# Kernel tuning notes

Hardware: AMD Instinct MI355X
Metric: run time of the kernel (lower is better)

The kernel has to match this reference:

```python
import jax, jax.numpy as jnp
import numpy as np

N_NODES = 50000
N_EDGES = 800000
NODE_IN = 256
EDGE_OUT = 64
GLOBAL_IN = 128
NODE_OUT = 256
HIDDEN = 512
N_GRAPHS = 64


def setup_inputs() -> dict:
    key = jax.random.key(0)
    ks = jax.random.split(key, 8)
    x = jax.random.normal(ks[0], (N_NODES, NODE_IN), dtype=jnp.float32)
    edge_index = jax.random.randint(ks[1], (2, N_EDGES), 0, N_NODES, dtype=jnp.int64)
    edge_attr = jax.random.normal(ks[2], (N_EDGES, EDGE_OUT), dtype=jnp.float32)
    u = jax.random.normal(ks[3], (N_GRAPHS, GLOBAL_IN), dtype=jnp.float32)
    batch = jnp.sort(jax.random.randint(ks[4], (N_NODES,), 0, N_GRAPHS, dtype=jnp.int64))
    in_dim = NODE_IN + EDGE_OUT + GLOBAL_IN
    # MLP params (torch nn.Linear default init: U(-1/sqrt(fan_in), 1/sqrt(fan_in)))
    b1s = 1.0 / np.sqrt(in_dim)
    b2s = 1.0 / np.sqrt(HIDDEN)
    W1 = jax.random.uniform(ks[5], (in_dim, HIDDEN), dtype=jnp.float32, minval=-b1s, maxval=b1s)
    b1 = jnp.zeros((HIDDEN,), dtype=jnp.float32)
    W2 = jax.random.uniform(ks[6], (HIDDEN, NODE_OUT), dtype=jnp.float32, minval=-b2s, maxval=b2s)
    b2 = jnp.zeros((NODE_OUT,), dtype=jnp.float32)
    return {"x": x, "edge_index": edge_index, "edge_attr": edge_attr, "u": u,
            "batch": batch, "W1": W1, "b1": b1, "W2": W2, "b2": b2}


def reference(x, edge_index, edge_attr, u, batch, W1, b1, W2, b2):
    n = x.shape[0]
    src = edge_index[0]
    # scatter_mean(edge_attr, src, dim=0, dim_size=n)
    sums = jax.ops.segment_sum(edge_attr, src, num_segments=n)          # [N, E_out]
    counts = jax.ops.segment_sum(jnp.ones((edge_attr.shape[0],), edge_attr.dtype),
                                 src, num_segments=n)                   # [N]
    edge_attr_agg = sums / jnp.maximum(counts, 1.0)[:, None]
    u_expanded = u[batch]                                               # [N, G_in]
    combined = jnp.concatenate([x, edge_attr_agg, u_expanded], axis=1)  # [N, 448]
    h = jax.nn.relu(combined @ W1 + b1)                                 # [N, H]
    return h @ W2 + b2                                                  # [N, N_out]
```

## Files before the change

### kernel.cpp

```cpp
#include <hip/hip_runtime.h>
#include <hip/hip_bf16.h>
#include <stdint.h>

#define NN 50000
#define NE 800000
#define NODE_IN 256
#define EDGE_OUT 64
#define GLOBAL_IN 128
#define NODE_OUT 256
#define HIDDEN 512
#define K1 320
#define N_GRAPHS 64
#define MAXDEG 64

typedef __attribute__((ext_vector_type(8))) short bf16x8;
typedef __attribute__((ext_vector_type(4))) float f32x4;
typedef __attribute__((ext_vector_type(4))) unsigned short us4;

__device__ __forceinline__ unsigned short f2bf(float x) {
    union { float f; unsigned int u; } c; c.f = x;
    unsigned int u = c.u;
    unsigned int r = (u + 0x7FFFu + ((u >> 16) & 1u)) >> 16;
    return (unsigned short)r;
}

#define GLD_LDS(gp, lp) __builtin_amdgcn_global_load_lds( \
    (const __attribute__((address_space(1))) unsigned int*)(gp), \
    (__attribute__((address_space(3))) unsigned int*)(lp), 16, 0, 0)

#define PREP_W1 (HIDDEN * K1)
#define PREP_W2 (PREP_W1 + NODE_OUT * HIDDEN)
#define PREP_G  (PREP_W2 + N_GRAPHS * HIDDEN)
#define PREP_Z  (PREP_G + NN)
__global__ __launch_bounds__(256)
void prep(const float* __restrict__ W1, const float* __restrict__ W2,
          const float* __restrict__ u, const float* __restrict__ b1,
          unsigned short* __restrict__ W1T, unsigned short* __restrict__ W2T,
          float* __restrict__ G, int* __restrict__ cnt)
{
    int idx = blockIdx.x * 256 + threadIdx.x;
    if (idx < PREP_W1) {
        int n = idx / K1, k = idx - n * K1;
        W1T[idx] = f2bf(W1[(size_t)k * HIDDEN + n]);
    } else if (idx < PREP_W2) {
        int j = idx - PREP_W1;
        int n = j / HIDDEN, k = j - n * HIDDEN;
        W2T[j] = f2bf(W2[(size_t)k * NODE_OUT + n]);
    } else if (idx < PREP_G) {
        int j = idx - PREP_W2;
        int g = j >> 9, col = j & 511;
        const float* up = u + (size_t)g * GLOBAL_IN;
        float acc = b1[col];
        #pragma unroll 4
        for (int k = 0; k < GLOBAL_IN; ++k)
            acc += up[k] * W1[(size_t)(K1 + k) * HIDDEN + col];
        G[j] = acc;
    } else if (idx < PREP_Z) {
        cnt[idx - PREP_G] = 0;
    }
}

__global__ __launch_bounds__(256)
void fill_perm(const int* __restrict__ src, int* __restrict__ cnt,
               int* __restrict__ perm)
{
    int e = blockIdx.x * 256 + threadIdx.x;
    if (e < NE) {
        int s = src[e];
        int pos = atomicAdd(&cnt[s], 1);
        if (pos < MAXDEG) perm[(size_t)s * MAXDEG + pos] = e;
    }
}

__global__ __launch_bounds__(256)
void seg_comb(const float* __restrict__ edge_attr,
              const int* __restrict__ perm,
              const int* __restrict__ cnt,
              const float* __restrict__ x,
              unsigned short* __restrict__ comb)
{
    int node = blockIdx.x * 4 + (threadIdx.x >> 6);
    if (node >= NN) return;
    int lane = threadIdx.x & 63;
    unsigned short* crow = comb + (size_t)node * K1;

    {
        const float4 v = *(const float4*)(x + (size_t)node * NODE_IN + lane * 4);
        us4 o = { f2bf(v.x), f2bf(v.y), f2bf(v.z), f2bf(v.w) };
        *(us4*)(crow + lane * 4) = o;
    }
    int c = cnt[node];
    int cc = c < MAXDEG ? c : MAXDEG;
    int g = lane >> 4;
    int f = (lane & 15) * 4;
    const int* pbase = perm + (size_t)node * MAXDEG;
    float4 acc = make_float4(0.f, 0.f, 0.f, 0.f);
    for (int i = g; i < cc; i += 4) {
        int e = pbase[i];
        const float4 v = *(const float4*)(edge_attr + (size_t)e * EDGE_OUT + f);
        acc.x += v.x; acc.y += v.y; acc.z += v.z; acc.w += v.w;
    }
    #pragma unroll
    for (int off = 16; off < 64; off <<= 1) {
        acc.x += __shfl_xor(acc.x, off, 64);
        acc.y += __shfl_xor(acc.y, off, 64);
        acc.z += __shfl_xor(acc.z, off, 64);
        acc.w += __shfl_xor(acc.w, off, 64);
    }
    if (g == 0) {
        float inv = 1.0f / fmaxf((float)c, 1.0f);
        us4 o = { f2bf(acc.x * inv), f2bf(acc.y * inv),
                  f2bf(acc.z * inv), f2bf(acc.w * inv) };
        *(us4*)(crow + NODE_IN + f) = o;
    }
}

template<int EPI>
__global__ __launch_bounds__(256)
void gemm_bt_128(const unsigned short* __restrict__ A,
                 const unsigned short* __restrict__ B,
                 const float* __restrict__ bias,
                 const int* __restrict__ batch,
                 void* __restrict__ Cv,
                 int M, int N, int K)
{
    __shared__ unsigned short lA[128 * 32];
    __shared__ unsigned short lB[128 * 32];
    const int tid = threadIdx.x;
    const int w = tid >> 6, l = tid & 63;
    const int m0 = blockIdx.y * 128;
    const int n0 = blockIdx.x * 128;
    const int wr = w >> 1, wc = w & 1;

    f32x4 acc[4][4] = {};

    const int cA0 = w * 64 + l;
    const int cA1 = (w + 4) * 64 + l;
    const int rA0 = cA0 >> 2, kA0 = (cA0 & 3) * 8;
    const int rA1 = cA1 >> 2, kA1 = (cA1 & 3) * 8;
    int gr0 = m0 + rA0; if (gr0 >= M) gr0 = M - 1;
    int gr1 = m0 + rA1; if (gr1 >= M) gr1 = M - 1;
    const unsigned short* pA0 = A + (size_t)gr0 * K + kA0;
    const unsigned short* pA1 = A + (size_t)gr1 * K + kA1;
    const unsigned short* pB0 = B + (size_t)(n0 + rA0) * K + kA0;
    const unsigned short* pB1 = B + (size_t)(n0 + rA1) * K + kA1;

    for (int k0 = 0; k0 < K; k0 += 32) {
        GLD_LDS(pA0 + k0, &lA[(size_t)cA0 * 8]);
        GLD_LDS(pA1 + k0, &lA[(size_t)cA1 * 8]);
        GLD_LDS(pB0 + k0, &lB[(size_t)cA0 * 8]);
        GLD_LDS(pB1 + k0, &lB[(size_t)cA1 * 8]);
        __syncthreads();

        bf16x8 af[4], bfr[4];
        #pragma unroll
        for (int m = 0; m < 4; ++m)
            af[m] = *(const bf16x8*)&lA[(wr * 64 + m * 16 + (l & 15)) * 32 + (l >> 4) * 8];
        #pragma unroll
        for (int n = 0; n < 4; ++n)
            bfr[n] = *(const bf16x8*)&lB[(wc * 64 + n * 16 + (l & 15)) * 32 + (l >> 4) * 8];

        #pragma unroll
        for (int m = 0; m < 4; ++m)
            #pragma unroll
            for (int n = 0; n < 4; ++n)
                acc[m][n] = __builtin_amdgcn_mfma_f32_16x16x32_bf16(af[m], bfr[n], acc[m][n], 0, 0, 0);

        __syncthreads();
    }

    const int cbase = n0 + wc * 64 + (l & 15);
    const int rbase = m0 + wr * 64 + ((l >> 4) << 2);
    if (EPI == 0) {
        unsigned short* C = (unsigned short*)Cv;
        #pragma unroll
        for (int m = 0; m < 4; ++m) {
            #pragma unroll
            for (int j = 0; j < 4; ++j) {
                int row = rbase + m * 16 + j;
                if (row < M) {
                    const float* grow = bias + (size_t)batch[row] * HIDDEN;
                    #pragma unroll
                    for (int n = 0; n < 4; ++n) {
                        int c = cbase + n * 16;
                        float v = acc[m][n][j] + grow[c];
                        v = fmaxf(v, 0.0f);
                        C[(size_t)row * N + c] = f2bf(v);
                    }
                }
            }
        }
    } else {
        float* C = (float*)Cv;
        #pragma unroll
        for (int m = 0; m < 4; ++m) {
            #pragma unroll
            for (int j = 0; j < 4; ++j) {
                int row = rbase + m * 16 + j;
                if (row < M) {
                    #pragma unroll
                    for (int n = 0; n < 4; ++n) {
                        int c = cbase + n * 16;
                        C[(size_t)row * N + c] = acc[m][n][j] + bias[c];
                    }
                }
            }
        }
    }
}

extern "C" void kernel_launch(void* const* d_in, const int* in_sizes, int n_in,
                              void* d_out, int out_size, void* d_ws, size_t ws_size,
                              hipStream_t stream)
{
    const float* x         = (const float*)d_in[0];
    const int*   edge_idx  = (const int*)d_in[1];
    const float* edge_attr = (const float*)d_in[2];
    const float* u         = (const float*)d_in[3];
    const int*   batch     = (const int*)d_in[4];
    const float* W1        = (const float*)d_in[5];
    const float* b1        = (const float*)d_in[6];
    const float* W2        = (const float*)d_in[7];
    const float* b2        = (const float*)d_in[8];
    float* out = (float*)d_out;

    char* ws = (char*)d_ws;
    int*            cnt    = (int*)(ws);
    int*            perm   = (int*)(ws + 200704);
    unsigned short* comb   = (unsigned short*)(ws + 13000704);
    unsigned short* W1T    = (unsigned short*)(ws + 45000704);
    unsigned short* W2T    = (unsigned short*)(ws + 45328384);
    float*          G      = (float*)(ws + 45590528);
    unsigned short* h      = (unsigned short*)(ws + 45721600);

    prep<<<(PREP_Z + 255) / 256, 256, 0, stream>>>(W1, W2, u, b1, W1T, W2T, G, cnt);

    fill_perm<<<(NE + 255) / 256, 256, 0, stream>>>(edge_idx, cnt, perm);

    seg_comb<<<(NN + 3) / 4, 256, 0, stream>>>(edge_attr, perm, cnt, x, comb);

    gemm_bt_128<0><<<dim3(HIDDEN / 128, (NN + 127) / 128), 256, 0, stream>>>(
        comb, W1T, G, batch, h, NN, HIDDEN, K1);
    gemm_bt_128<1><<<dim3(NODE_OUT / 128, (NN + 127) / 128), 256, 0, stream>>>(
        h, W2T, b2, nullptr, out, NN, NODE_OUT, HIDDEN);
}
```

Before: 227.9 us.

## Fuse both MLP GEMMs into one kernel keeping hidden chunks in LDS

Result: slower. 279.6 us (+22.7%).

```diff
diff --git a/kernel.cpp b/kernel.cpp
--- a/kernel.cpp
+++ b/kernel.cpp
@@ -12,6 +12,7 @@
 #define K1 320
 #define N_GRAPHS 64
 #define MAXDEG 64
+#define HCH_LD 136
 
 typedef __attribute__((ext_vector_type(8))) short bf16x8;
 typedef __attribute__((ext_vector_type(4))) float f32x4;
@@ -115,24 +116,24 @@
     }
 }
 
-template<int EPI>
-__global__ __launch_bounds__(256)
-void gemm_bt_128(const unsigned short* __restrict__ A,
-                 const unsigned short* __restrict__ B,
-                 const float* __restrict__ bias,
-                 const int* __restrict__ batch,
-                 void* __restrict__ Cv,
-                 int M, int N, int K)
+__global__ __launch_bounds__(256, 2)
+void mlp_fused(const unsigned short* __restrict__ A,
+               const unsigned short* __restrict__ B1,
+               const unsigned short* __restrict__ B2,
+               const float* __restrict__ G,
+               const int* __restrict__ batch,
+               const float* __restrict__ bias2,
+               float* __restrict__ out, int M)
 {
     __shared__ unsigned short lA[128 * 32];
     __shared__ unsigned short lB[128 * 32];
+    __shared__ unsigned short lW2[256 * 32];
+    __shared__ unsigned short hch[128 * HCH_LD];
+
     const int tid = threadIdx.x;
     const int w = tid >> 6, l = tid & 63;
-    const int m0 = blockIdx.y * 128;
-    const int n0 = blockIdx.x * 128;
     const int wr = w >> 1, wc = w & 1;
-
-    f32x4 acc[4][4] = {};
+    const int m0 = blockIdx.x * 128;
 
     const int cA0 = w * 64 + l;
     const int cA1 = (w + 4) * 64 + l;
@@ -140,69 +141,101 @@
     const int rA1 = cA1 >> 2, kA1 = (cA1 & 3) * 8;
     int gr0 = m0 + rA0; if (gr0 >= M) gr0 = M - 1;
     int gr1 = m0 + rA1; if (gr1 >= M) gr1 = M - 1;
-    const unsigned short* pA0 = A + (size_t)gr0 * K + kA0;
-    const unsigned short* pA1 = A + (size_t)gr1 * K + kA1;
-    const unsigned short* pB0 = B + (size_t)(n0 + rA0) * K + kA0;
-    const unsigned short* pB1 = B + (size_t)(n0 + rA1) * K + kA1;
-
-    for (int k0 = 0; k0 < K; k0 += 32) {
-        GLD_LDS(pA0 + k0, &lA[(size_t)cA0 * 8]);
-        GLD_LDS(pA1 + k0, &lA[(size_t)cA1 * 8]);
-        GLD_LDS(pB0 + k0, &lB[(size_t)cA0 * 8]);
-        GLD_LDS(pB1 + k0, &lB[(size_t)cA1 * 8]);
-        __syncthreads();
-
-        bf16x8 af[4], bfr[4];
-        #pragma unroll
-        for (int m = 0; m < 4; ++m)
-            af[m] = *(const bf16x8*)&lA[(wr * 64 + m * 16 + (l & 15)) * 32 + (l >> 4) * 8];
-        #pragma unroll
-        for (int n = 0; n < 4; ++n)
-            bfr[n] = *(const bf16x8*)&lB[(wc * 64 + n * 16 + (l & 15)) * 32 + (l >> 4) * 8];
-
-        #pragma unroll
-        for (int m = 0; m < 4; ++m)
+    const unsigned short* pA0 = A + (size_t)gr0 * K1 + kA0;
+    const unsigned short* pA1 = A + (size_t)gr1 * K1 + kA1;
+
+    const int cW0 = w * 64 + l;
+
+    f32x4 acc2[4][8] = {};
+
+    const int lrow = wr * 64 + (l & 15);
+    const int lko  = (l >> 4) * 8;
+
+    for (int cc = 0; cc < 4; ++cc) {
+        f32x4 acc1[4][4] = {};
+        const unsigned short* pB0 = B1 + (size_t)(cc * 128 + rA0) * K1 + kA0;
+        const unsigned short* pB1b = B1 + (size_t)(cc * 128 + rA1) * K1 + kA1;
+        for (int k0 = 0; k0 < K1; k0 += 32) {
+            GLD_LDS(pA0 + k0, &lA[(size_t)cA0 * 8]);
+            GLD_LDS(pA1 + k0, &lA[(size_t)cA1 * 8]);
+            GLD_LDS(pB0 + k0, &lB[(size_t)cA0 * 8]);
+            GLD_LDS(pB1b + k0, &lB[(size_t)cA1 * 8]);
+            __syncthreads();
+            bf16x8 af[4], bfr[4];
+            #pragma unroll
+            for (int m = 0; m < 4; ++m)
+                af[m] = *(const bf16x8*)&lA[(wr * 64 + m * 16 + (l & 15)) * 32 + lko];
             #pragma unroll
             for (int n = 0; n < 4; ++n)
-                acc[m][n] = __builtin_amdgcn_mfma_f32_16x16x32_bf16(af[m], bfr[n], acc[m][n], 0, 0, 0);
-
-        __syncthreads();
-    }
-
-    const int cbase = n0 + wc * 64 + (l & 15);
-    const int rbase = m0 + wr * 64 + ((l >> 4) << 2);
-    if (EPI == 0) {
-        unsigned short* C = (unsigned short*)Cv;
-        #pragma unroll
-        for (int m = 0; m < 4; ++m) {
-            #pragma unroll
-            for (int j = 0; j < 4; ++j) {
-                int row = rbase + m * 16 + j;
-                if (row < M) {
-                    const float* grow = bias + (size_t)batch[row] * HIDDEN;
+                bfr[n] = *(const bf16x8*)&lB[(wc * 64 + n * 16 + (l & 15)) * 32 + lko];
+            #pragma unroll
+            for (int m = 0; m < 4; ++m)
+                #pragma unroll
+                for (int n = 0; n < 4; ++n)
+                    acc1[m][n] = __builtin_amdgcn_mfma_f32_16x16x32_bf16(af[m], bfr[n], acc1[m][n], 0, 0, 0);
+            __syncthreads();
+        }
+
+        {
+            const int colb = wc * 64 + (l & 15);
+            const int rowb = wr * 64 + ((l >> 4) << 2);
+            #pragma unroll
+            for (int m = 0; m < 4; ++m) {
+                #pragma unroll
+                for (int j = 0; j < 4; ++j) {
+                    int lr = rowb + m * 16 + j;
+                    int grow = m0 + lr; if (grow >= M) grow = M - 1;
+                    const float* gp = G + (size_t)batch[grow] * HIDDEN + cc * 128;
                     #pragma unroll
                     for (int n = 0; n < 4; ++n) {
-                        int c = cbase + n * 16;
-                        float v = acc[m][n][j] + grow[c];
-                        v = fmaxf(v, 0.0f);
-                        C[(size_t)row * N + c] = f2bf(v);
+                        int col = colb + n * 16;
+                        float v = acc1[m][n][j] + gp[col];
+                        hch[lr * HCH_LD + col] = f2bf(fmaxf(v, 0.0f));
                     }
                 }
             }
         }
-    } else {
-        float* C = (float*)Cv;
+
+        for (int k2 = 0; k2 < 128; k2 += 32) {
+            #pragma unroll
+            for (int i = 0; i < 4; ++i) {
+                int c = cW0 + i * 256;
+                int rw = c >> 2, ko = (c & 3) * 8;
+                GLD_LDS(B2 + (size_t)rw * HIDDEN + cc * 128 + k2 + ko, &lW2[(size_t)c * 8]);
+            }
+            __syncthreads();
+            bf16x8 am[4];
+            #pragma unroll
+            for (int m = 0; m < 4; ++m)
+                am[m] = *(const bf16x8*)&hch[(wr * 64 + m * 16 + (l & 15)) * HCH_LD + lko + k2];
+            #pragma unroll
+            for (int h = 0; h < 2; ++h) {
+                bf16x8 bn[4];
+                #pragma unroll
+                for (int n = 0; n < 4; ++n)
+                    bn[n] = *(const bf16x8*)&lW2[(wc * 128 + h * 64 + n * 16 + (l & 15)) * 32 + lko];
+                #pragma unroll
+                for (int m = 0; m < 4; ++m)
+                    #pragma unroll
+                    for (int n = 0; n < 4; ++n)
+                        acc2[m][h * 4 + n] = __builtin_amdgcn_mfma_f32_16x16x32_bf16(am[m], bn[n], acc2[m][h * 4 + n], 0, 0, 0);
+            }
+            __syncthreads();
+        }
+    }
+
+    const int cbase = wc * 128 + (l & 15);
+    const int rbase = m0 + wr * 64 + ((l >> 4) << 2);
+    #pragma unroll
+    for (int m = 0; m < 4; ++m) {
         #pragma unroll
-        for (int m = 0; m < 4; ++m) {
-            #pragma unroll
-            for (int j = 0; j < 4; ++j) {
-                int row = rbase + m * 16 + j;
-                if (row < M) {
-                    #pragma unroll
-                    for (int n = 0; n < 4; ++n) {
-                        int c = cbase + n * 16;
-                        C[(size_t)row * N + c] = acc[m][n][j] + bias[c];
-                    }
+        for (int j = 0; j < 4; ++j) {
+            int row = rbase + m * 16 + j;
+            if (row < M) {
+                #pragma unroll
+                for (int nn = 0; nn < 8; ++nn) {
+                    int col = cbase + nn * 16;
+                    out[(size_t)row * NODE_OUT + col] = acc2[m][nn][j] + bias2[col];
                 }
             }
         }
@@ -231,7 +264,6 @@
     unsigned short* W1T    = (unsigned short*)(ws + 45000704);
     unsigned short* W2T    = (unsigned short*)(ws + 45328384);
     float*          G      = (float*)(ws + 45590528);
-    unsigned short* h      = (unsigned short*)(ws + 45721600);
 
     prep<<<(PREP_Z + 255) / 256, 256, 0, stream>>>(W1, W2, u, b1, W1T, W2T, G, cnt);
 
@@ -239,8 +271,6 @@
 
     seg_comb<<<(NN + 3) / 4, 256, 0, stream>>>(edge_attr, perm, cnt, x, comb);
 
-    gemm_bt_128<0><<<dim3(HIDDEN / 128, (NN + 127) / 128), 256, 0, stream>>>(
-        comb, W1T, G, batch, h, NN, HIDDEN, K1);
-    gemm_bt_128<1><<<dim3(NODE_OUT / 128, (NN + 127) / 128), 256, 0, stream>>>(
-        h, W2T, b2, nullptr, out, NN, NODE_OUT, HIDDEN);
-}
+    mlp_fused<<<(NN + 127) / 128, 256, 0, stream>>>(
+        comb, W1T, W2T, G, batch, b2, out, NN);
+}
```
